# Performance work log

Measured on AMD Instinct MI355X. Metric: run time of the kernel, lower is better.

## Reference

```python
import jax, jax.numpy as jnp
import numpy as np

B, L, D = 32, 512, 128          # batch, seq_len, d_model (= num graph nodes N)
E, HS, DTR, U = 64, 64, 4, 32   # d_proj_E, d_proj_H (state), dt_rank, d_proj_U
R, K, DE, NH = 3, 3, 10, 4      # mamba layers, cheb order, d_e, heads
EPS = 1e-5


def _ln(x, g, b):
    m = jnp.mean(x, -1, keepdims=True)
    v = jnp.mean((x - m) ** 2, -1, keepdims=True)
    return (x - m) / jnp.sqrt(v + EPS) * g + b


def _mamba(x, in_w, conv_w, conv_b, xproj_w, dt_w, dt_b, Alog, Dp, out_w):
    b, l, _ = x.shape
    xz = x @ in_w                                  # (b,l,2E)
    xp, res = xz[..., :E], xz[..., E:]
    xc = jnp.transpose(xp, (0, 2, 1))              # (b,E,l)
    # causal depthwise conv: torch pads both sides by d_conv-1 then slices [:l]
    xc = jax.lax.conv_general_dilated(
        xc, conv_w, (1,), [(conv_w.shape[-1] - 1, 0)],
        dimension_numbers=('NCH', 'OIH', 'NCH'), feature_group_count=E)
    xc = xc + conv_b[None, :, None]
    xp = jax.nn.silu(jnp.transpose(xc, (0, 2, 1)))  # (b,l,E)
    xdbl = xp @ xproj_w                             # (b,l,DTR+2*HS)
    delta = jax.nn.softplus(xdbl[..., :DTR] @ dt_w + dt_b)        # (b,l,E)
    Bm = xdbl[..., DTR:DTR + HS]                                   # (b,l,HS)
    Cm = xdbl[..., DTR + HS:]                                      # (b,l,HS)
    A = -jnp.exp(Alog)                                             # (E,HS)
    dA = jnp.exp(delta[..., None] * A)                             # (b,l,E,HS)
    dBu = delta[..., None] * Bm[:, :, None, :] * xp[..., None]     # (b,l,E,HS)

    def step(s, t):
        dA_t, dBu_t, C_t = t
        s = dA_t * s + dBu_t
        return s, jnp.einsum('bdn,bn->bd', s, C_t)

    _, ys = jax.lax.scan(step, jnp.zeros((b, E, HS), x.dtype),
                         (jnp.swapaxes(dA, 0, 1), jnp.swapaxes(dBu, 0, 1),
                          jnp.swapaxes(Cm, 0, 1)))
    y = jnp.swapaxes(ys, 0, 1) + xp * Dp
    y = y * jax.nn.sigmoid(res)
    return y @ out_w


def _forward(x, mb_in_w, mb_conv_w, mb_conv_b, mb_xproj_w, mb_dt_w, mb_dt_b,
             mb_Alog, mb_D, mb_out_w, ln1_g, ln1_b, ln2_g, ln2_b,
             ffn_w1, ffn_b1, ffn_w2, ffn_b2,
             psi_emb, psi, W_q, W_k, attn_alpha, F_w, f_b, head_mix,
             head_w, head_b):
    # ---- bidirectional Mamba stack ----
    for i in range(R):
        f, bk = 2 * i, 2 * i + 1
        Y1 = _mamba(x, mb_in_w[f], mb_conv_w[f], mb_conv_b[f], mb_xproj_w[f],
                    mb_dt_w[f], mb_dt_b[f], mb_Alog[f], mb_D[f], mb_out_w[f])
        Y2 = jnp.flip(_mamba(jnp.flip(x, 1), mb_in_w[bk], mb_conv_w[bk],
                             mb_conv_b[bk], mb_xproj_w[bk], mb_dt_w[bk],
                             mb_dt_b[bk], mb_Alog[bk], mb_D[bk], mb_out_w[bk]), 1)
        Y3 = _ln(x + Y1 + Y2, ln1_g[i], ln1_b[i])
        Yp = jax.nn.relu(Y3 @ ffn_w1[i] + ffn_b1[i]) @ ffn_w2[i] + ffn_b2[i]
        x = _ln(Yp + Y3, ln2_g[i], ln2_b[i])
    h = jnp.transpose(x, (0, 2, 1))                # (B, N=D, L)
    # ---- MAGAC (deterministic single MC sample, eval, no edge drop) ----
    diff = psi_emb[:, None, :] - psi_emb[None, :, :]
    A_g = jax.nn.softmax(jnp.exp(-psi * jnp.sum(diff * diff, -1)), axis=1)
    Q = jnp.einsum('nd,dhm->nhm', psi_emb, W_q)
    Kt = jnp.einsum('nd,dhm->nhm', psi_emb, W_k)
    attn = jax.nn.softmax(jnp.einsum('nhd,mhd->hnm', Q, Kt)
                          / jnp.sqrt(jnp.asarray(DE, x.dtype)), axis=-1)
    alpha = jax.nn.sigmoid(attn_alpha)
    A_effs = alpha * A_g[None] + (1.0 - alpha) * attn   # (H,N,N)
    mix = jax.nn.softmax(head_mix)
    I = jnp.eye(D, dtype=x.dtype)
    out = jnp.zeros((x.shape[0], D), x.dtype)
    for hh in range(NH):
        A = A_effs[hh]
        sup = [I, A]
        for _ in range(2, K + 1):
            sup.append(2.0 * A @ sup[-1] - sup[-2])
        S = jnp.stack(sup, 0)                             # (K+1,N,N)
        Wf = jnp.einsum('nd,dkl->nkl', psi_emb, F_w[hh])  # (N,K+1,L)
        bf = psi_emb @ f_b[hh]                            # (N,)
        out_h = jnp.einsum('knm,bml,nkl->bn', S, h, Wf) + bf
        out = out + mix[hh] * out_h
    log_var = jnp.zeros_like(out)
    pred = out @ head_w + head_b                          # (B,1)
    return pred, log_var


def setup_inputs() -> dict:
    key = jax.random.key(0)
    ks = iter(jax.random.split(key, 40))
    nrm = lambda shp, s=0.05: (jax.random.normal(next(ks), shp, jnp.float32) * s)
    M = 2 * R
    base_Alog = jnp.log(jnp.arange(1, HS + 1, dtype=jnp.float32))
    inp = {
        'x': jax.random.normal(next(ks), (B, L, D), jnp.float32),
        'mb_in_w': nrm((M, D, 2 * E)),
        'mb_conv_w': nrm((M, E, 1, 3), 0.2),
        'mb_conv_b': jnp.zeros((M, E), jnp.float32),
        'mb_xproj_w': nrm((M, E, DTR + 2 * HS)),
        'mb_dt_w': nrm((M, DTR, E), 0.2),
        'mb_dt_b': jnp.zeros((M, E), jnp.float32),
        'mb_Alog': jnp.tile(base_Alog[None, None, :], (M, E, 1)),
        'mb_D': jnp.ones((M, E), jnp.float32),
        'mb_out_w': nrm((M, E, D)),
        'ln1_g': jnp.ones((R, D), jnp.float32),
        'ln1_b': jnp.zeros((R, D), jnp.float32),
        'ln2_g': jnp.ones((R, D), jnp.float32),
        'ln2_b': jnp.zeros((R, D), jnp.float32),
        'ffn_w1': nrm((R, D, U)),
        'ffn_b1': jnp.zeros((R, U), jnp.float32),
        'ffn_w2': nrm((R, U, D)),
        'ffn_b2': jnp.zeros((R, D), jnp.float32),
        'psi_emb': jax.random.normal(next(ks), (D, DE), jnp.float32),
        'psi': jnp.asarray(1.0, jnp.float32),
        'W_q': jax.random.normal(next(ks), (DE, NH, DE), jnp.float32),
        'W_k': jax.random.normal(next(ks), (DE, NH, DE), jnp.float32),
        'attn_alpha': jnp.asarray(0.5, jnp.float32),
        'F_w': nrm((NH, DE, K + 1, L), 0.05),
        'f_b': nrm((NH, DE), 1.0),
        'head_mix': jnp.ones((NH,), jnp.float32),
        'head_w': nrm((D, 1)),
        'head_b': jnp.zeros((1,), jnp.float32),
    }
    return inp


def reference(x, mb_in_w, mb_conv_w, mb_conv_b, mb_xproj_w, mb_dt_w, mb_dt_b,
              mb_Alog, mb_D, mb_out_w, ln1_g, ln1_b, ln2_g, ln2_b,
              ffn_w1, ffn_b1, ffn_w2, ffn_b2,
              psi_emb, psi, W_q, W_k, attn_alpha, F_w, f_b, head_mix,
              head_w, head_b):
    return _forward(x, mb_in_w, mb_conv_w, mb_conv_b, mb_xproj_w, mb_dt_w,
                    mb_dt_b, mb_Alog, mb_D, mb_out_w, ln1_g, ln1_b, ln2_g,
                    ln2_b, ffn_w1, ffn_b1, ffn_w2, ffn_b2, psi_emb, psi,
                    W_q, W_k, attn_alpha, F_w, f_b, head_mix, head_w, head_b)
```

## Files before the change

kernel.cpp:

```cpp
#include <hip/hip_runtime.h>
#include <hip/hip_bf16.h>


#define B_ 32
#define L_ 512
#define D_ 128
#define E_ 64
#define HS_ 64

#define OFF_X     0u
#define OFF_XZF   2097152u
#define OFF_XZB   4194304u
#define OFF_XPF   6291456u
#define OFF_XPB   7340032u
#define OFF_PKF   8388608u
#define OFF_PKB   10485760u
#define OFF_XBCF  12582912u
#define OFF_XBCB  14680064u
#define OFF_YSF   16777216u
#define OFF_YSB   17825792u
#define OFF_V     2097152u
#define OFF_WFT   10485760u
#define OFF_STT   11534336u
#define OFF_AEFF  11796480u
#define OFF_PART  12582912u
#define OFF_RED1  16777216u

__device__ __forceinline__ float sigf(float x) { return 1.f / (1.f + __expf(-x)); }
__device__ __forceinline__ unsigned int bf16r(float x) {
    unsigned int u = __float_as_uint(x);
    return (u + 0x7fffu + ((u >> 16) & 1u)) >> 16;
}

__global__ __launch_bounds__(256) void gemm_in2_kernel(
    const float* __restrict__ X, const float* __restrict__ WF, const float* __restrict__ WB,
    float* __restrict__ xzF, float* __restrict__ xzB)
{
    __shared__ float sxT[128][36];
    __shared__ float sw[2][16][128];
    const int tid = threadIdx.x;
    const int r0 = blockIdx.x * 32;
    for (int q = tid; q < 1024; q += 256) {
        const int r = q >> 5, k4 = q & 31;
        const float4 v = *(const float4*)&X[(size_t)(r0 + r) * 128 + k4 * 4];
        sxT[k4 * 4 + 0][r] = v.x; sxT[k4 * 4 + 1][r] = v.y;
        sxT[k4 * 4 + 2][r] = v.z; sxT[k4 * 4 + 3][r] = v.w;
    }
    const int wv = tid >> 6, lane = tid & 63;
    const int d = wv >> 1, ch = wv & 1;
    const int r4 = lane >> 4, c16 = lane & 15;
    float4 acc[8];
#pragma unroll
    for (int j = 0; j < 8; ++j) acc[j] = float4{0.f, 0.f, 0.f, 0.f};
    for (int ko = 0; ko < 128; ko += 16) {
        __syncthreads();
        for (int q = tid; q < 1024; q += 256) {
            const int dd = q >> 9, kk = (q >> 5) & 15, c4 = q & 31;
            *(float4*)&sw[dd][kk][c4 * 4] =
                *(const float4*)&((dd ? WB : WF)[(ko + kk) * 128 + c4 * 4]);
        }
        __syncthreads();
#pragma unroll
        for (int kk = 0; kk < 16; ++kk) {
            const float4 w4 = *(const float4*)&sw[d][kk][ch * 64 + c16 * 4];
            const float4 xa = *(const float4*)&sxT[ko + kk][r4 * 8];
            const float4 xb = *(const float4*)&sxT[ko + kk][r4 * 8 + 4];
            const float xs[8] = {xa.x, xa.y, xa.z, xa.w, xb.x, xb.y, xb.z, xb.w};
#pragma unroll
            for (int j = 0; j < 8; ++j) {
                acc[j].x = fmaf(xs[j], w4.x, acc[j].x);
                acc[j].y = fmaf(xs[j], w4.y, acc[j].y);
                acc[j].z = fmaf(xs[j], w4.z, acc[j].z);
                acc[j].w = fmaf(xs[j], w4.w, acc[j].w);
            }
        }
    }
    float* xz = d ? xzB : xzF;
#pragma unroll
    for (int j = 0; j < 8; ++j) {
        *(float4*)&xz[(r0 + r4 * 8 + j) * 128 + ch * 64 + c16 * 4] = acc[j];
    }
}

__global__ __launch_bounds__(256) void prep4_kernel(
    const float* __restrict__ xzF_, const float* __restrict__ xzB_,
    const float* __restrict__ conv_w, const float* __restrict__ conv_b,
    const float* __restrict__ xproj_w, const float* __restrict__ dt_w,
    const float* __restrict__ dt_b, int layer,
    float* __restrict__ xpF_, float* __restrict__ xpB_,
    unsigned int* __restrict__ xbcF_, unsigned int* __restrict__ xbcB_,
    float* __restrict__ pkF_, float* __restrict__ pkB_)
{
    __shared__ float sW[8448];
    __shared__ float sxp4[4][64][4];
    __shared__ float sdl4[4][4][4];
    const int tid = threadIdx.x, wv = tid >> 6, lane = tid & 63;
    const int dir = (int)(blockIdx.x >= 1024);
    const int r0 = (blockIdx.x & 1023) * 16;
    const int b = r0 >> 9;
    const int m = layer * 2 + dir;
    const float* Wg = xproj_w + m * 8448;
    for (int q = tid; q < 2112; q += 256) ((float4*)sW)[q] = ((const float4*)Wg)[q];
    const float* xz = dir ? xzB_ : xzF_;
    float* xp  = dir ? xpB_  : xpF_;
    unsigned int* xbc = dir ? xbcB_ : xbcF_;
    float* pkx = dir ? pkB_  : pkF_;
    const float* cw = conv_w + m * 192 + lane * 3;
    const float cw0 = cw[0], cw1 = cw[1], cw2 = cw[2];
    const float cb  = conv_b[m * 64 + lane];
    const float dtb = dt_b[m * 64 + lane];
    const float* dwp = dt_w + m * 256;
    const float dw0 = dwp[lane], dw1 = dwp[64 + lane], dw2 = dwp[128 + lane], dw3 = dwp[192 + lane];
    float uu[4];
#pragma unroll
    for (int it = 0; it < 4; ++it) {
        const int row = r0 + wv * 4 + it;
        const int l = row & 511;
        const int l1 = dir ? l + 1 : l - 1;
        const int l2 = dir ? l + 2 : l - 2;
        float acc = cb;
        const float x0 = xz[(size_t)row * 128 + lane];
        const float x1 = (l1 >= 0 && l1 < 512) ? xz[(size_t)(b * 512 + l1) * 128 + lane] : 0.f;
        const float x2 = (l2 >= 0 && l2 < 512) ? xz[(size_t)(b * 512 + l2) * 128 + lane] : 0.f;
        acc += cw0 * x2 + cw1 * x1 + cw2 * x0;
        const float u = acc * sigf(acc);
        xp[row * 64 + lane] = u;
        uu[it] = u;
    }
    *(float4*)&sxp4[wv][lane][0] = float4{uu[0], uu[1], uu[2], uu[3]};
    __syncthreads();
    const int jdt = lane & 3;
    float aB[4] = {0.f, 0.f, 0.f, 0.f};
    float aC[4] = {0.f, 0.f, 0.f, 0.f};
    float adt[4] = {0.f, 0.f, 0.f, 0.f};
#pragma unroll 4
    for (int k = 0; k < 64; ++k) {
        const float wB = sW[k * 132 + 4 + lane];
        const float wC = sW[k * 132 + 68 + lane];
        const float wd = sW[k * 132 + jdt];
        const float4 xv = *(const float4*)&sxp4[wv][k][0];
        aB[0] = fmaf(xv.x, wB, aB[0]); aC[0] = fmaf(xv.x, wC, aC[0]); adt[0] = fmaf(xv.x, wd, adt[0]);
        aB[1] = fmaf(xv.y, wB, aB[1]); aC[1] = fmaf(xv.y, wC, aC[1]); adt[1] = fmaf(xv.y, wd, adt[1]);
        aB[2] = fmaf(xv.z, wB, aB[2]); aC[2] = fmaf(xv.z, wC, aC[2]); adt[2] = fmaf(xv.z, wd, adt[2]);
        aB[3] = fmaf(xv.w, wB, aB[3]); aC[3] = fmaf(xv.w, wC, aC[3]); adt[3] = fmaf(xv.w, wd, adt[3]);
    }
#pragma unroll
    for (int it = 0; it < 4; ++it) {
        const int row = r0 + wv * 4 + it;
        xbc[row * 64 + lane] = (bf16r(aC[it]) << 16) | bf16r(aB[it]);
        if (lane < 4) sdl4[wv][it][lane] = adt[it];
    }
#pragma unroll
    for (int it = 0; it < 4; ++it) {
        const int row = r0 + wv * 4 + it;
        float dpre = fmaf(sdl4[wv][it][0], dw0, dtb);
        dpre = fmaf(sdl4[wv][it][1], dw1, dpre);
        dpre = fmaf(sdl4[wv][it][2], dw2, dpre);
        dpre = fmaf(sdl4[wv][it][3], dw3, dpre);
        const float dlt = (dpre > 20.f) ? dpre : log1pf(__expf(dpre));
        ((float2*)pkx)[row * 64 + lane] = float2{dlt, dlt * uu[it]};
    }
}

__global__ __launch_bounds__(256, 4) void scan8_kernel(
    const unsigned int* __restrict__ xbcF, const unsigned int* __restrict__ xbcB,
    const float* __restrict__ pkF, const float* __restrict__ pkB,
    const float* __restrict__ AlogF, const float* __restrict__ AlogB,
    float* __restrict__ ysF, float* __restrict__ ysB)
{
    __shared__ unsigned int sbc[2][1024];
    __shared__ float spk[2][4][16][2];
    __shared__ float ytile[4][16][68];
    const int tid = threadIdx.x, wv = tid >> 6, lane = tid & 63;
    const int bx = blockIdx.x;
    const int db = bx & 63;
    const int dir = db >> 5;
    const int b   = db & 31;
    const int e0  = (bx >> 6) * 4;
    const int e   = e0 + wv;
    const unsigned int* xbc = dir ? xbcB : xbcF;
    const float* pk  = dir ? pkB  : pkF;
    const float* Aw  = dir ? AlogB : AlogF;
    float* ys = dir ? ysB : ysF;
    const float a2 = -__expf(Aw[e * 64 + lane]) * 1.4426950408889634f;
    float s = 0.f;
    float* yrow = ys + (size_t)(b * 64 + e) * 512;

    const int psl = tid & 15, pw_ = tid >> 4;

#define STG_LOAD(RS)                                                              \
    {                                                                             \
        nb = *(const uint4*)(xbc + (size_t)(RS) * 64 + tid * 4);                  \
        if (tid < 64)                                                             \
            npp = *(const float2*)(pk + (size_t)((RS) + psl) * 128 + (e0 + pw_) * 2); \
    }
#define STG_WRITE(BUF)                                                            \
    {                                                                             \
        *(uint4*)(&sbc[BUF][tid * 4]) = nb;                                       \
        if (tid < 64) *(float2*)(&spk[BUF][pw_][psl][0]) = npp;                   \
    }

#define SCAN16(REV)                                                               \
    {                                                                             \
        const unsigned int* bc = &sbc[cur][0];                                    \
        const float* pq = &spk[cur][wv][0][0];                                    \
        _Pragma("unroll")                                                         \
        for (int j = 0; j < 8; ++j) {                                             \
            const int pj = (REV) ? 7 - j : j;                                     \
            const float4 pk4 = *(const float4*)(pq + pj * 4);                     \
            const int sA = (REV) ? 15 - 2 * j : 2 * j;                            \
            const int sB = (REV) ? 14 - 2 * j : 2 * j + 1;                        \
            const float dlA = (REV) ? pk4.z : pk4.x;                              \
            const float duA = (REV) ? pk4.w : pk4.y;                              \
            const float dlB = (REV) ? pk4.x : pk4.z;                              \
            const float duB = (REV) ? pk4.y : pk4.w;                              \
            const unsigned int bA = bc[sA * 64 + lane];                           \
            const float BnA = __uint_as_float(bA << 16);                          \
            const float CnA = __uint_as_float(bA & 0xffff0000u);                  \
            s = fmaf(__builtin_amdgcn_exp2f(dlA * a2), s, duA * BnA);             \
            ytile[wv][2 * j][lane] = s * CnA;                                     \
            const unsigned int bB = bc[sB * 64 + lane];                           \
            const float BnB = __uint_as_float(bB << 16);                          \
            const float CnB = __uint_as_float(bB & 0xffff0000u);                  \
            s = fmaf(__builtin_amdgcn_exp2f(dlB * a2), s, duB * BnB);             \
            ytile[wv][2 * j + 1][lane] = s * CnB;                                 \
        }                                                                         \
    }

    {
        uint4 nb; float2 npp;
        const int rs0 = b * 512 + (dir ? 496 : 0);
        STG_LOAD(rs0);
        STG_WRITE(0);
    }
    __syncthreads();

    int cur = 0;
    const int rr = lane & 15, sg = lane >> 4;
    for (int t = 0; t < 32; ++t) {
        uint4 nb; float2 npp;
        const bool more = (t + 1) < 32;
        if (more) {
            const int rs = b * 512 + (dir ? (496 - (t + 1) * 16) : ((t + 1) * 16));
            STG_LOAD(rs);
        }
        if (dir == 0) { SCAN16(0) } else { SCAN16(1) }
        {
            const float* yt = &ytile[wv][rr][sg * 16];
            const float4 A0 = *(const float4*)yt;
            const float4 A1 = *(const float4*)(yt + 4);
            const float4 A2 = *(const float4*)(yt + 8);
            const float4 A3 = *(const float4*)(yt + 12);
            float p = ((A0.x + A0.y) + (A0.z + A0.w)) + ((A1.x + A1.y) + (A1.z + A1.w))
                    + ((A2.x + A2.y) + (A2.z + A2.w)) + ((A3.x + A3.y) + (A3.z + A3.w));
            p += __shfl_xor(p, 16);
            p += __shfl_xor(p, 32);
            if (lane < 16) {
                const int lg = dir ? (511 - (t * 16 + rr)) : (t * 16 + rr);
                yrow[lg] = p;
            }
        }
        if (more) STG_WRITE(cur ^ 1);
        __syncthreads();
        cur ^= 1;
    }
#undef STG_LOAD
#undef STG_WRITE
#undef SCAN16
}

__global__ __launch_bounds__(256) void opfn2_kernel(
    const float* __restrict__ ysF, const float* __restrict__ ysB,
    const float* __restrict__ xpF, const float* __restrict__ xpB,
    const float* __restrict__ xzF, const float* __restrict__ xzB,
    const float* __restrict__ Dp, int layer,
    const float* __restrict__ Xc, const float* __restrict__ out_w,
    const float* __restrict__ W1, const float* __restrict__ b1,
    const float* __restrict__ W2, const float* __restrict__ b2,
    const float* __restrict__ g1, const float* __restrict__ bb1,
    const float* __restrict__ g2, const float* __restrict__ bb2,
    float* __restrict__ xout,
    const float* __restrict__ WFn, const float* __restrict__ WBn,
    float* __restrict__ xzFo, float* __restrict__ xzBo)
{
    __shared__ float smem[8832];
    float* syt = smem;
    float* y3  = smem;
    float* sy  = smem + 2176;
    float* sw  = smem + 4224;
    float* sh  = smem + 8320;
    const int tid = threadIdx.x;
    const int r0 = blockIdx.x * 16;
    const int b = r0 >> 9, l0 = r0 & 511;

    for (int q = tid; q < 512; q += 256) {
        const int d = q >> 8, ee = (q >> 2) & 63, rq = q & 3;
        const float* ysp = d ? ysB : ysF;
        const float4 v = *(const float4*)&ysp[(size_t)(b * 64 + ee) * 512 + l0 + rq * 4];
        float* dst = &syt[(d * 64 + ee) * 17 + rq * 4];
        dst[0] = v.x; dst[1] = v.y; dst[2] = v.z; dst[3] = v.w;
    }
    __syncthreads();
    for (int q = tid; q < 2048; q += 256) {
        const int r = q >> 7, c = q & 127;
        const int d = c >> 6, ee = c & 63;
        const int row = r0 + r;
        const float dv  = Dp[(layer * 2 + d) * 64 + ee];
        const float u   = (d ? xpB : xpF)[(size_t)row * 64 + ee];
        const float res = (d ? xzB : xzF)[(size_t)row * 128 + 64 + ee];
        sy[r * 128 + c] = (syt[(d * 64 + ee) * 17 + r] + u * dv) * sigf(res);
    }
    const int wv = tid >> 6, lane = tid & 63;
    const float* WFp = out_w + (layer * 2) * 8192;
    const float* WBp = out_w + (layer * 2 + 1) * 8192;
    float acc[4][2];
#pragma unroll
    for (int r = 0; r < 4; ++r) { acc[r][0] = 0.f; acc[r][1] = 0.f; }
    for (int ko = 0; ko < 128; ko += 32) {
        __syncthreads();
        for (int q = tid; q < 1024; q += 256) {
            const int kk = q >> 5, c4 = q & 31;
            const int kg = ko + kk;
            *(float4*)&sw[kk * 128 + c4 * 4] = (kg < 64)
                ? *(const float4*)&WFp[kg * 128 + c4 * 4]
                : *(const float4*)&WBp[(kg - 64) * 128 + c4 * 4];
        }
        __syncthreads();
#define OPSTEP(SRC, COMP, J)                                                      \
        {                                                                         \
            const float w0 = sw[(kk + (J)) * 128 + lane];                         \
            const float w1 = sw[(kk + (J)) * 128 + lane + 64];                    \
            acc[0][0] = fmaf(y40.COMP, w0, acc[0][0]);                            \
            acc[0][1] = fmaf(y40.COMP, w1, acc[0][1]);                            \
            acc[1][0] = fmaf(y41.COMP, w0, acc[1][0]);                            \
            acc[1][1] = fmaf(y41.COMP, w1, acc[1][1]);                            \
            acc[2][0] = fmaf(y42.COMP, w0, acc[2][0]);                            \
            acc[2][1] = fmaf(y42.COMP, w1, acc[2][1]);                            \
            acc[3][0] = fmaf(y43.COMP, w0, acc[3][0]);                            \
            acc[3][1] = fmaf(y43.COMP, w1, acc[3][1]);                            \
        }
#pragma unroll
        for (int kk = 0; kk < 32; kk += 4) {
            const float4 y40 = *(const float4*)&sy[(wv * 4 + 0) * 128 + ko + kk];
            const float4 y41 = *(const float4*)&sy[(wv * 4 + 1) * 128 + ko + kk];
            const float4 y42 = *(const float4*)&sy[(wv * 4 + 2) * 128 + ko + kk];
            const float4 y43 = *(const float4*)&sy[(wv * 4 + 3) * 128 + ko + kk];
            OPSTEP(sy, x, 0) OPSTEP(sy, y, 1) OPSTEP(sy, z, 2) OPSTEP(sy, w, 3)
        }
    }
    __syncthreads();
    for (int q = tid; q < 1024; q += 256) ((float4*)sw)[q] = ((const float4*)W1)[q];
#pragma unroll
    for (int r = 0; r < 4; ++r) {
        const int rl = wv * 4 + r;
        const int row = r0 + rl;
        float v0 = acc[r][0] + Xc[(size_t)row * 128 + lane];
        float v1 = acc[r][1] + Xc[(size_t)row * 128 + lane + 64];
        float sum = v0 + v1, sq = v0 * v0 + v1 * v1;
#pragma unroll
        for (int o = 32; o >= 1; o >>= 1) { sum += __shfl_xor(sum, o); sq += __shfl_xor(sq, o); }
        const float mean = sum * (1.f / 128.f);
        const float var = sq * (1.f / 128.f) - mean * mean;
        const float rs = rsqrtf(var + 1e-5f);
        y3[rl * 128 + lane]      = (v0 - mean) * rs * g1[lane] + bb1[lane];
        y3[rl * 128 + lane + 64] = (v1 - mean) * rs * g1[lane + 64] + bb1[lane + 64];
    }
    __syncthreads();
    {
        const int r = tid >> 4, u = tid & 15;
        float h0 = b1[u], h1 = b1[u + 16];
#pragma unroll 8
        for (int k = 0; k < 128; ++k) {
            const float xv = y3[r * 128 + k];
            h0 = fmaf(xv, sw[k * 32 + u], h0);
            h1 = fmaf(xv, sw[k * 32 + u + 16], h1);
        }
        sh[r * 32 + u]      = fmaxf(h0, 0.f);
        sh[r * 32 + u + 16] = fmaxf(h1, 0.f);
    }
    __syncthreads();
    for (int q = tid; q < 1024; q += 256) ((float4*)sw)[q] = ((const float4*)W2)[q];
    __syncthreads();
    float xr[4][2];
#pragma unroll
    for (int r = 0; r < 4; ++r) {
        const int rl = wv * 4 + r;
        float a0 = b2[lane], a1 = b2[lane + 64];
#pragma unroll 8
        for (int k = 0; k < 32; ++k) {
            const float hv = sh[rl * 32 + k];
            a0 = fmaf(hv, sw[k * 128 + lane], a0);
            a1 = fmaf(hv, sw[k * 128 + lane + 64], a1);
        }
        const float v0 = a0 + y3[rl * 128 + lane];
        const float v1 = a1 + y3[rl * 128 + lane + 64];
        float sum = v0 + v1, sq = v0 * v0 + v1 * v1;
#pragma unroll
        for (int o = 32; o >= 1; o >>= 1) { sum += __shfl_xor(sum, o); sq += __shfl_xor(sq, o); }
        const float mean = sum * (1.f / 128.f);
        const float var = sq * (1.f / 128.f) - mean * mean;
        const float rs = rsqrtf(var + 1e-5f);
        const int row = r0 + rl;
        const float o0 = (v0 - mean) * rs * g2[lane] + bb2[lane];
        const float o1 = (v1 - mean) * rs * g2[lane + 64] + bb2[lane + 64];
        xout[(size_t)row * 128 + lane]      = o0;
        xout[(size_t)row * 128 + lane + 64] = o1;
        xr[r][0] = o0; xr[r][1] = o1;
    }
    if (WFn == nullptr) return;
    __syncthreads();
    float* sxr = y3;
#pragma unroll
    for (int r = 0; r < 4; ++r) {
        sxr[(wv * 4 + r) * 128 + lane]      = xr[r][0];
        sxr[(wv * 4 + r) * 128 + lane + 64] = xr[r][1];
    }
    for (int d = 0; d < 2; ++d) {
        const float* Wn = d ? WBn : WFn;
        float* xzo = d ? xzBo : xzFo;
#pragma unroll
        for (int r = 0; r < 4; ++r) { acc[r][0] = 0.f; acc[r][1] = 0.f; }
        for (int ko = 0; ko < 128; ko += 32) {
            __syncthreads();
            for (int q = tid; q < 1024; q += 256) {
                const int kk = q >> 5, c4 = q & 31;
                *(float4*)&sw[kk * 128 + c4 * 4] = *(const float4*)&Wn[(ko + kk) * 128 + c4 * 4];
            }
            __syncthreads();
#pragma unroll
            for (int kk = 0; kk < 32; kk += 4) {
                const float4 y40 = *(const float4*)&sxr[(wv * 4 + 0) * 128 + ko + kk];
                const float4 y41 = *(const float4*)&sxr[(wv * 4 + 1) * 128 + ko + kk];
                const float4 y42 = *(const float4*)&sxr[(wv * 4 + 2) * 128 + ko + kk];
                const float4 y43 = *(const float4*)&sxr[(wv * 4 + 3) * 128 + ko + kk];
                OPSTEP(sxr, x, 0) OPSTEP(sxr, y, 1) OPSTEP(sxr, z, 2) OPSTEP(sxr, w, 3)
            }
        }
#pragma unroll
        for (int r = 0; r < 4; ++r) {
            const int row = r0 + wv * 4 + r;
            xzo[(size_t)row * 128 + lane]      = acc[r][0];
            xzo[(size_t)row * 128 + lane + 64] = acc[r][1];
        }
    }
#undef OPSTEP
}

__global__ __launch_bounds__(256) void head_wfqk_kernel(
    const float* __restrict__ psi, const float* __restrict__ F_w, float* __restrict__ WfT,
    const float* __restrict__ psis, const float* __restrict__ W_q, const float* __restrict__ W_k,
    const float* __restrict__ attn_a,
    float* __restrict__ Aeff, float* __restrict__ StT)
{
    __shared__ float sQ[2][10];
    __shared__ float red[2][128];
    if (blockIdx.x < 4096) {
        const int idx = blockIdx.x * 256 + threadIdx.x;
        const int n = idx & 127, l = (idx >> 7) & 511, k = (idx >> 16) & 3, h = idx >> 18;
        float acc = 0.f;
#pragma unroll
        for (int d = 0; d < 10; ++d)
            acc = fmaf(psi[n * 10 + d], F_w[((h * 10 + d) * 4 + k) * 512 + l], acc);
        WfT[idx] = acc;
        return;
    }
    const int q = blockIdx.x - 4096;
    const int half = threadIdx.x >> 7, mcol = threadIdx.x & 127;
    const int unit = q * 2 + half;
    const int h = unit >> 7, n = unit & 127;
    float Kreg[10];
#pragma unroll
    for (int d = 0; d < 10; ++d) Kreg[d] = 0.f;
#pragma unroll
    for (int d0 = 0; d0 < 10; ++d0) {
        const float pv = psi[mcol * 10 + d0];
#pragma unroll
        for (int d = 0; d < 10; ++d) Kreg[d] = fmaf(pv, W_k[(d0 * 4 + h) * 10 + d], Kreg[d]);
    }
    if (mcol < 10) {
        float qd = 0.f;
        for (int d0 = 0; d0 < 10; ++d0)
            qd = fmaf(psi[n * 10 + d0], W_q[(d0 * 4 + h) * 10 + mcol], qd);
        sQ[half][mcol] = qd;
    }
    __syncthreads();
    float d2 = 0.f;
#pragma unroll
    for (int d = 0; d < 10; ++d) { const float df = psi[n * 10 + d] - psi[mcol * 10 + d]; d2 = fmaf(df, df, d2); }
    const float gv = __expf(-psis[0] * d2);
    float qv = 0.f;
#pragma unroll
    for (int d = 0; d < 10; ++d) qv = fmaf(sQ[half][d], Kreg[d], qv);
    qv *= 0.3162277660168379332f;
    float* rd = red[half];
    float r;
    rd[mcol] = gv; __syncthreads();
    for (int s = 64; s >= 1; s >>= 1) { if (mcol < s) rd[mcol] = fmaxf(rd[mcol], rd[mcol + s]); __syncthreads(); }
    r = rd[0]; __syncthreads();
    const float eg = __expf(gv - r);
    rd[mcol] = eg; __syncthreads();
    for (int s = 64; s >= 1; s >>= 1) { if (mcol < s) rd[mcol] += rd[mcol + s]; __syncthreads(); }
    const float gsum = rd[0]; __syncthreads();
    rd[mcol] = qv; __syncthreads();
    for (int s = 64; s >= 1; s >>= 1) { if (mcol < s) rd[mcol] = fmaxf(rd[mcol], rd[mcol + s]); __syncthreads(); }
    r = rd[0]; __syncthreads();
    const float eq = __expf(qv - r);
    rd[mcol] = eq; __syncthreads();
    for (int s = 64; s >= 1; s >>= 1) { if (mcol < s) rd[mcol] += rd[mcol + s]; __syncthreads(); }
    const float qsum = rd[0];
    const float al = sigf(attn_a[0]);
    const float aeff = al * (eg / gsum) + (1.f - al) * (eq / qsum);
    Aeff[h * 16384 + n * 128 + mcol] = aeff;
    StT[((h * 4 + 1) * 128 + mcol) * 128 + n] = aeff;
    StT[((h * 4 + 0) * 128 + mcol) * 128 + n] = (mcol == n) ? 1.f : 0.f;
}

__global__ __launch_bounds__(256) void head_cheb_kernel(
    const float* __restrict__ Aeff, float* __restrict__ StT, int kk)
{
    const int h = blockIdx.x >> 6;
    const int m0 = ((blockIdx.x & 63) << 1) + (threadIdx.x >> 7);
    const int n = threadIdx.x & 127;
    const float* Ar = Aeff + h * 16384 + n * 128;
    const float* Sp = StT + ((h * 4 + kk - 1) * 128 + m0) * 128;
    float acc = 0.f;
#pragma unroll 8
    for (int p = 0; p < 128; ++p) acc = fmaf(Ar[p], Sp[p], acc);
    const float s2 = StT[((h * 4 + kk - 2) * 128 + m0) * 128 + n];
    StT[((h * 4 + kk) * 128 + m0) * 128 + n] = 2.f * acc - s2;
}

__global__ __launch_bounds__(256) void head_v4_kernel(
    const float* __restrict__ StT, const float* __restrict__ WfT, const float* __restrict__ hmix,
    float* __restrict__ V)
{
    const float m0 = hmix[0], m1 = hmix[1], m2 = hmix[2], m3 = hmix[3];
    const float mxx = fmaxf(fmaxf(m0, m1), fmaxf(m2, m3));
    const float e0 = __expf(m0 - mxx), e1 = __expf(m1 - mxx), e2 = __expf(m2 - mxx), e3 = __expf(m3 - mxx);
    const float inv = 1.f / (e0 + e1 + e2 + e3);
    const float mixv[4] = {e0 * inv, e1 * inv, e2 * inv, e3 * inv};
    const int tid = threadIdx.x;
    const int lt = blockIdx.x & 63, mm = blockIdx.x >> 6;
    const int n4 = tid & 31, mh = tid >> 5;
    const int m = mm * 8 + mh;
    const int l0 = lt * 8, n0 = n4 * 4;
    float4 sv[16];
#pragma unroll
    for (int h = 0; h < 4; ++h) {
        const float mx = mixv[h];
#pragma unroll
        for (int k = 0; k < 4; ++k) {
            const float4 v = *(const float4*)&StT[(size_t)((h * 4 + k) * 128 + m) * 128 + n0];
            sv[h * 4 + k] = float4{v.x * mx, v.y * mx, v.z * mx, v.w * mx};
        }
    }
#pragma unroll
    for (int j = 0; j < 8; ++j) {
        const int l = l0 + j;
        float4 acc = {0.f, 0.f, 0.f, 0.f};
#pragma unroll
        for (int hk = 0; hk < 16; ++hk) {
            const float4 w = *(const float4*)&WfT[(size_t)(hk * 512 + l) * 128 + n0];
            acc.x = fmaf(sv[hk].x, w.x, acc.x);
            acc.y = fmaf(sv[hk].y, w.y, acc.y);
            acc.z = fmaf(sv[hk].z, w.z, acc.z);
            acc.w = fmaf(sv[hk].w, w.w, acc.w);
        }
        *(float4*)&V[(size_t)(l * 128 + m) * 128 + n0] = acc;
    }
}

__global__ __launch_bounds__(256) void head_ctr_kernel(
    const float* __restrict__ Xf, const float* __restrict__ V, float* __restrict__ partial)
{
    __shared__ float sx[32][128];
    const int l = blockIdx.x, tid = threadIdx.x;
    const int n = tid & 127, mh = tid >> 7;
    for (int q = tid; q < 1024; q += 256) {
        const int b = q >> 5, m4 = q & 31;
        *(float4*)&sx[b][m4 * 4] = *(const float4*)&Xf[(size_t)(b * 512 + l) * 128 + m4 * 4];
    }
    __syncthreads();
    float acc[32];
#pragma unroll
    for (int b = 0; b < 32; ++b) acc[b] = 0.f;
    const float* vp = V + (size_t)(l * 128 + mh * 64) * 128 + n;
    for (int mm = 0; mm < 64; ++mm) {
        const float v = vp[(size_t)mm * 128];
        const int m = mh * 64 + mm;
#pragma unroll
        for (int b = 0; b < 32; ++b) acc[b] = fmaf(sx[b][m], v, acc[b]);
    }
#pragma unroll
    for (int b = 0; b < 32; ++b)
        partial[(size_t)((l * 2 + mh) * 32 + b) * 128 + n] = acc[b];
}

__global__ __launch_bounds__(128) void head_red_kernel(
    const float* __restrict__ partial, float* __restrict__ red1)
{
    const int b = blockIdx.x >> 5, cs = blockIdx.x & 31, n = threadIdx.x;
    const float* p = partial + ((size_t)(cs * 32) * 32 + b) * 128 + n;
    float s = 0.f;
#pragma unroll 8
    for (int c = 0; c < 32; ++c) s += p[(size_t)c * 4096];
    red1[(b * 32 + cs) * 128 + n] = s;
}

__global__ __launch_bounds__(128) void head_out_kernel(
    const float* __restrict__ red1, const float* __restrict__ psi,
    const float* __restrict__ f_b, const float* __restrict__ hmix,
    const float* __restrict__ head_w, const float* __restrict__ head_b, float* __restrict__ out)
{
    __shared__ float red[128];
    const int b = blockIdx.x, n = threadIdx.x;
    const float m0 = hmix[0], m1 = hmix[1], m2 = hmix[2], m3 = hmix[3];
    const float mxx = fmaxf(fmaxf(m0, m1), fmaxf(m2, m3));
    const float e0 = __expf(m0 - mxx), e1 = __expf(m1 - mxx), e2 = __expf(m2 - mxx), e3 = __expf(m3 - mxx);
    const float inv = 1.f / (e0 + e1 + e2 + e3);
    const float mixv[4] = {e0 * inv, e1 * inv, e2 * inv, e3 * inv};
    float s = 0.f;
#pragma unroll
    for (int h = 0; h < 4; ++h) {
        float t = 0.f;
#pragma unroll
        for (int d = 0; d < 10; ++d) t = fmaf(psi[n * 10 + d], f_b[h * 10 + d], t);
        s = fmaf(mixv[h], t, s);
    }
#pragma unroll 8
    for (int cs = 0; cs < 32; ++cs) s += red1[(b * 32 + cs) * 128 + n];
    red[n] = s * head_w[n];
    __syncthreads();
    for (int st = 64; st >= 1; st >>= 1) { if (n < st) red[n] += red[n + st]; __syncthreads(); }
    if (n == 0) out[b] = red[0] + head_b[0];
    out[32 + b * 128 + n] = 0.f;
}

extern "C" void kernel_launch(void* const* d_in, const int* in_sizes, int n_in,
                              void* d_out, int out_size, void* d_ws, size_t ws_size,
                              hipStream_t stream) {
    const float* x_in    = (const float*)d_in[0];
    const float* in_w    = (const float*)d_in[1];
    const float* conv_w  = (const float*)d_in[2];
    const float* conv_b  = (const float*)d_in[3];
    const float* xproj_w = (const float*)d_in[4];
    const float* dt_w    = (const float*)d_in[5];
    const float* dt_b    = (const float*)d_in[6];
    const float* Alog    = (const float*)d_in[7];
    const float* Dp      = (const float*)d_in[8];
    const float* out_w   = (const float*)d_in[9];
    const float* ln1_g   = (const float*)d_in[10];
    const float* ln1_b   = (const float*)d_in[11];
    const float* ln2_g   = (const float*)d_in[12];
    const float* ln2_b   = (const float*)d_in[13];
    const float* ffn_w1  = (const float*)d_in[14];
    const float* ffn_b1  = (const float*)d_in[15];
    const float* ffn_w2  = (const float*)d_in[16];
    const float* ffn_b2  = (const float*)d_in[17];
    const float* psi_emb = (const float*)d_in[18];
    const float* psi_s   = (const float*)d_in[19];
    const float* W_q     = (const float*)d_in[20];
    const float* W_k     = (const float*)d_in[21];
    const float* attn_a  = (const float*)d_in[22];
    const float* F_w     = (const float*)d_in[23];
    const float* f_b     = (const float*)d_in[24];
    const float* hmix    = (const float*)d_in[25];
    const float* head_w  = (const float*)d_in[26];
    const float* head_b  = (const float*)d_in[27];
    float* ws = (float*)d_ws;
    float* outp = (float*)d_out;

    gemm_in2_kernel<<<512, 256, 0, stream>>>(
        x_in, in_w, in_w + 16384, ws + OFF_XZF, ws + OFF_XZB);
    for (int i = 0; i < 3; ++i) {
        const float* xcur = (i == 0) ? x_in : (ws + OFF_X);
        const int mF = 2 * i, mB = 2 * i + 1;
        prep4_kernel<<<2048, 256, 0, stream>>>(
            ws + OFF_XZF, ws + OFF_XZB, conv_w, conv_b, xproj_w, dt_w, dt_b, i,
            ws + OFF_XPF, ws + OFF_XPB,
            (unsigned int*)(ws + OFF_XBCF), (unsigned int*)(ws + OFF_XBCB),
            ws + OFF_PKF, ws + OFF_PKB);
        scan8_kernel<<<1024, 256, 0, stream>>>(
            (const unsigned int*)(ws + OFF_XBCF), (const unsigned int*)(ws + OFF_XBCB),
            ws + OFF_PKF, ws + OFF_PKB,
            Alog + mF * 4096, Alog + mB * 4096, ws + OFF_YSF, ws + OFF_YSB);
        const float* WFn = (i < 2) ? (in_w + (2 * i + 2) * 16384) : nullptr;
        const float* WBn = (i < 2) ? (in_w + (2 * i + 3) * 16384) : nullptr;
        opfn2_kernel<<<1024, 256, 0, stream>>>(
            ws + OFF_YSF, ws + OFF_YSB, ws + OFF_XPF, ws + OFF_XPB, ws + OFF_XZF, ws + OFF_XZB,
            Dp, i, xcur, out_w,
            ffn_w1 + i * 4096, ffn_b1 + i * 32, ffn_w2 + i * 4096, ffn_b2 + i * 128,
            ln1_g + i * 128, ln1_b + i * 128, ln2_g + i * 128, ln2_b + i * 128,
            ws + OFF_X, WFn, WBn, ws + OFF_XZF, ws + OFF_XZB);
    }
    head_wfqk_kernel<<<4352, 256, 0, stream>>>(
        psi_emb, F_w, ws + OFF_WFT, psi_s, W_q, W_k, attn_a,
        ws + OFF_AEFF, ws + OFF_STT);
    head_cheb_kernel<<<256, 256, 0, stream>>>(ws + OFF_AEFF, ws + OFF_STT, 2);
    head_cheb_kernel<<<256, 256, 0, stream>>>(ws + OFF_AEFF, ws + OFF_STT, 3);
    head_v4_kernel<<<1024, 256, 0, stream>>>(ws + OFF_STT, ws + OFF_WFT, hmix, ws + OFF_V);
    head_ctr_kernel<<<512, 256, 0, stream>>>(ws + OFF_X, ws + OFF_V, ws + OFF_PART);
    head_red_kernel<<<1024, 128, 0, stream>>>(ws + OFF_PART, ws + OFF_RED1);
    head_out_kernel<<<32, 128, 0, stream>>>(
        ws + OFF_RED1, psi_emb, f_b, hmix, head_w, head_b, outp);
}
```

Baseline: 506.1 us.

## Process 32 rows per block in fused out-proj/FFN kernel to halve weight reloads

The fused out-projection, LayerNorm, FFN and next-layer in-projection kernel now handles 32 rows per block instead of 16, so each wave computes 8 rows and every weight tile staged in shared memory is reused twice as much. The launch drops from 1024 to 512 blocks. The gating prologue is fused into a single pass, the FFN first layer gives each thread 4 outputs, and the two next-layer GEMMs are merged into one chunk loop. The cost is more registers per thread (a 16-entry accumulator with an occupancy hint of 4), fewer blocks to spread across CUs, and slightly more shared memory. The scan kernel also gets small index rewrites.

```diff
diff --git a/kernel.cpp b/kernel.cpp
--- a/kernel.cpp
+++ b/kernel.cpp
@@ -218,12 +218,12 @@
             const float BnA = __uint_as_float(bA << 16);                          \
             const float CnA = __uint_as_float(bA & 0xffff0000u);                  \
             s = fmaf(__builtin_amdgcn_exp2f(dlA * a2), s, duA * BnA);             \
-            ytile[wv][2 * j][lane] = s * CnA;                                     \
+            ytile[wv][sA][lane] = s * CnA;                                        \
             const unsigned int bB = bc[sB * 64 + lane];                           \
             const float BnB = __uint_as_float(bB << 16);                          \
             const float CnB = __uint_as_float(bB & 0xffff0000u);                  \
             s = fmaf(__builtin_amdgcn_exp2f(dlB * a2), s, duB * BnB);             \
-            ytile[wv][2 * j + 1][lane] = s * CnB;                                 \
+            ytile[wv][sB][lane] = s * CnB;                                        \
         }                                                                         \
     }
 
@@ -256,7 +256,7 @@
             p += __shfl_xor(p, 16);
             p += __shfl_xor(p, 32);
             if (lane < 16) {
-                const int lg = dir ? (511 - (t * 16 + rr)) : (t * 16 + rr);
+                const int lg = dir ? (496 + rr - t * 16) : (t * 16 + rr);
                 yrow[lg] = p;
             }
         }
@@ -269,7 +269,7 @@
 #undef SCAN16
 }
 
-__global__ __launch_bounds__(256) void opfn2_kernel(
+__global__ __launch_bounds__(256, 4) void opfn3_kernel(
     const float* __restrict__ ysF, const float* __restrict__ ysB,
     const float* __restrict__ xpF, const float* __restrict__ xpB,
     const float* __restrict__ xzF, const float* __restrict__ xzB,
@@ -283,76 +283,82 @@
     const float* __restrict__ WFn, const float* __restrict__ WBn,
     float* __restrict__ xzFo, float* __restrict__ xzBo)
 {
-    __shared__ float smem[8832];
-    float* syt = smem;
-    float* y3  = smem;
-    float* sy  = smem + 2176;
-    float* sw  = smem + 4224;
-    float* sh  = smem + 8320;
+    __shared__ float smem[9216];
+    float* syy = smem;
+    float* sw  = smem + 4096;
+    float* sh  = smem + 8192;
     const int tid = threadIdx.x;
-    const int r0 = blockIdx.x * 16;
+    const int r0 = blockIdx.x * 32;
     const int b = r0 >> 9, l0 = r0 & 511;
-
-    for (int q = tid; q < 512; q += 256) {
-        const int d = q >> 8, ee = (q >> 2) & 63, rq = q & 3;
-        const float* ysp = d ? ysB : ysF;
-        const float4 v = *(const float4*)&ysp[(size_t)(b * 64 + ee) * 512 + l0 + rq * 4];
-        float* dst = &syt[(d * 64 + ee) * 17 + rq * 4];
-        dst[0] = v.x; dst[1] = v.y; dst[2] = v.z; dst[3] = v.w;
-    }
-    __syncthreads();
-    for (int q = tid; q < 2048; q += 256) {
-        const int r = q >> 7, c = q & 127;
-        const int d = c >> 6, ee = c & 63;
-        const int row = r0 + r;
-        const float dv  = Dp[(layer * 2 + d) * 64 + ee];
-        const float u   = (d ? xpB : xpF)[(size_t)row * 64 + ee];
-        const float res = (d ? xzB : xzF)[(size_t)row * 128 + 64 + ee];
-        sy[r * 128 + c] = (syt[(d * 64 + ee) * 17 + r] + u * dv) * sigf(res);
-    }
     const int wv = tid >> 6, lane = tid & 63;
     const float* WFp = out_w + (layer * 2) * 8192;
     const float* WBp = out_w + (layer * 2 + 1) * 8192;
-    float acc[4][2];
-#pragma unroll
-    for (int r = 0; r < 4; ++r) { acc[r][0] = 0.f; acc[r][1] = 0.f; }
-    for (int ko = 0; ko < 128; ko += 32) {
-        __syncthreads();
+
+    for (int q = tid; q < 1024; q += 256) {
+        const int d = q >> 9, ee = (q >> 3) & 63, rq = q & 7;
+        const float* ysp = d ? ysB : ysF;
+        const float4 v = *(const float4*)&ysp[(size_t)(b * 64 + ee) * 512 + l0 + rq * 4];
+        const float dv = Dp[(layer * 2 + d) * 64 + ee];
+        const float* xpp = d ? xpB : xpF;
+        const float* xzp = d ? xzB : xzF;
+        const float vv[4] = {v.x, v.y, v.z, v.w};
+#pragma unroll
+        for (int j = 0; j < 4; ++j) {
+            const int r = rq * 4 + j;
+            const int row = r0 + r;
+            const float u   = xpp[(size_t)row * 64 + ee];
+            const float res = xzp[(size_t)row * 128 + 64 + ee];
+            syy[r * 128 + d * 64 + ee] = (vv[j] + u * dv) * sigf(res);
+        }
+    }
+    __syncthreads();
+
+    float acc[8][2];
+#pragma unroll
+    for (int r = 0; r < 8; ++r) { acc[r][0] = 0.f; acc[r][1] = 0.f; }
+#define OPSTEP8(COMP, J)                                                          \
+        {                                                                         \
+            const float w0 = sw[(kk + (J)) * 128 + lane];                         \
+            const float w1 = sw[(kk + (J)) * 128 + lane + 64];                    \
+            acc[0][0] = fmaf(y40.COMP, w0, acc[0][0]); acc[0][1] = fmaf(y40.COMP, w1, acc[0][1]); \
+            acc[1][0] = fmaf(y41.COMP, w0, acc[1][0]); acc[1][1] = fmaf(y41.COMP, w1, acc[1][1]); \
+            acc[2][0] = fmaf(y42.COMP, w0, acc[2][0]); acc[2][1] = fmaf(y42.COMP, w1, acc[2][1]); \
+            acc[3][0] = fmaf(y43.COMP, w0, acc[3][0]); acc[3][1] = fmaf(y43.COMP, w1, acc[3][1]); \
+            acc[4][0] = fmaf(y44.COMP, w0, acc[4][0]); acc[4][1] = fmaf(y44.COMP, w1, acc[4][1]); \
+            acc[5][0] = fmaf(y45.COMP, w0, acc[5][0]); acc[5][1] = fmaf(y45.COMP, w1, acc[5][1]); \
+            acc[6][0] = fmaf(y46.COMP, w0, acc[6][0]); acc[6][1] = fmaf(y46.COMP, w1, acc[6][1]); \
+            acc[7][0] = fmaf(y47.COMP, w0, acc[7][0]); acc[7][1] = fmaf(y47.COMP, w1, acc[7][1]); \
+        }
+#define GEMM_CHUNK8(SRC, KO)                                                      \
+    _Pragma("unroll")                                                             \
+    for (int kk = 0; kk < 32; kk += 4) {                                          \
+        const float4 y40 = *(const float4*)&(SRC)[(wv * 8 + 0) * 128 + (KO) + kk];\
+        const float4 y41 = *(const float4*)&(SRC)[(wv * 8 + 1) * 128 + (KO) + kk];\
+        const float4 y42 = *(const float4*)&(SRC)[(wv * 8 + 2) * 128 + (KO) + kk];\
+        const float4 y43 = *(const float4*)&(SRC)[(wv * 8 + 3) * 128 + (KO) + kk];\
+        const float4 y44 = *(const float4*)&(SRC)[(wv * 8 + 4) * 128 + (KO) + kk];\
+        const float4 y45 = *(const float4*)&(SRC)[(wv * 8 + 5) * 128 + (KO) + kk];\
+        const float4 y46 = *(const float4*)&(SRC)[(wv * 8 + 6) * 128 + (KO) + kk];\
+        const float4 y47 = *(const float4*)&(SRC)[(wv * 8 + 7) * 128 + (KO) + kk];\
+        OPSTEP8(x, 0) OPSTEP8(y, 1) OPSTEP8(z, 2) OPSTEP8(w, 3)                  \
+    }
+    for (int koi = 0; koi < 4; ++koi) {
+        if (koi) __syncthreads();
         for (int q = tid; q < 1024; q += 256) {
             const int kk = q >> 5, c4 = q & 31;
-            const int kg = ko + kk;
+            const int kg = koi * 32 + kk;
             *(float4*)&sw[kk * 128 + c4 * 4] = (kg < 64)
                 ? *(const float4*)&WFp[kg * 128 + c4 * 4]
                 : *(const float4*)&WBp[(kg - 64) * 128 + c4 * 4];
         }
         __syncthreads();
-#define OPSTEP(SRC, COMP, J)                                                      \
-        {                                                                         \
-            const float w0 = sw[(kk + (J)) * 128 + lane];                         \
-            const float w1 = sw[(kk + (J)) * 128 + lane + 64];                    \
-            acc[0][0] = fmaf(y40.COMP, w0, acc[0][0]);                            \
-            acc[0][1] = fmaf(y40.COMP, w1, acc[0][1]);                            \
-            acc[1][0] = fmaf(y41.COMP, w0, acc[1][0]);                            \
-            acc[1][1] = fmaf(y41.COMP, w1, acc[1][1]);                            \
-            acc[2][0] = fmaf(y42.COMP, w0, acc[2][0]);                            \
-            acc[2][1] = fmaf(y42.COMP, w1, acc[2][1]);                            \
-            acc[3][0] = fmaf(y43.COMP, w0, acc[3][0]);                            \
-            acc[3][1] = fmaf(y43.COMP, w1, acc[3][1]);                            \
-        }
-#pragma unroll
-        for (int kk = 0; kk < 32; kk += 4) {
-            const float4 y40 = *(const float4*)&sy[(wv * 4 + 0) * 128 + ko + kk];
-            const float4 y41 = *(const float4*)&sy[(wv * 4 + 1) * 128 + ko + kk];
-            const float4 y42 = *(const float4*)&sy[(wv * 4 + 2) * 128 + ko + kk];
-            const float4 y43 = *(const float4*)&sy[(wv * 4 + 3) * 128 + ko + kk];
-            OPSTEP(sy, x, 0) OPSTEP(sy, y, 1) OPSTEP(sy, z, 2) OPSTEP(sy, w, 3)
-        }
+        GEMM_CHUNK8(syy, koi * 32);
     }
     __syncthreads();
     for (int q = tid; q < 1024; q += 256) ((float4*)sw)[q] = ((const float4*)W1)[q];
 #pragma unroll
-    for (int r = 0; r < 4; ++r) {
-        const int rl = wv * 4 + r;
+    for (int r = 0; r < 8; ++r) {
+        const int rl = wv * 8 + r;
         const int row = r0 + rl;
         float v0 = acc[r][0] + Xc[(size_t)row * 128 + lane];
         float v1 = acc[r][1] + Xc[(size_t)row * 128 + lane + 64];
@@ -362,29 +368,33 @@
         const float mean = sum * (1.f / 128.f);
         const float var = sq * (1.f / 128.f) - mean * mean;
         const float rs = rsqrtf(var + 1e-5f);
-        y3[rl * 128 + lane]      = (v0 - mean) * rs * g1[lane] + bb1[lane];
-        y3[rl * 128 + lane + 64] = (v1 - mean) * rs * g1[lane + 64] + bb1[lane + 64];
+        syy[rl * 128 + lane]      = (v0 - mean) * rs * g1[lane] + bb1[lane];
+        syy[rl * 128 + lane + 64] = (v1 - mean) * rs * g1[lane + 64] + bb1[lane + 64];
     }
     __syncthreads();
     {
-        const int r = tid >> 4, u = tid & 15;
-        float h0 = b1[u], h1 = b1[u + 16];
+        const int r = tid >> 3, ug = (tid & 7) * 4;
+        float h0 = b1[ug], h1 = b1[ug + 1], h2 = b1[ug + 2], h3 = b1[ug + 3];
 #pragma unroll 8
         for (int k = 0; k < 128; ++k) {
-            const float xv = y3[r * 128 + k];
-            h0 = fmaf(xv, sw[k * 32 + u], h0);
-            h1 = fmaf(xv, sw[k * 32 + u + 16], h1);
-        }
-        sh[r * 32 + u]      = fmaxf(h0, 0.f);
-        sh[r * 32 + u + 16] = fmaxf(h1, 0.f);
+            const float xv = syy[r * 128 + k];
+            h0 = fmaf(xv, sw[k * 32 + ug], h0);
+            h1 = fmaf(xv, sw[k * 32 + ug + 1], h1);
+            h2 = fmaf(xv, sw[k * 32 + ug + 2], h2);
+            h3 = fmaf(xv, sw[k * 32 + ug + 3], h3);
+        }
+        sh[r * 32 + ug]     = fmaxf(h0, 0.f);
+        sh[r * 32 + ug + 1] = fmaxf(h1, 0.f);
+        sh[r * 32 + ug + 2] = fmaxf(h2, 0.f);
+        sh[r * 32 + ug + 3] = fmaxf(h3, 0.f);
     }
     __syncthreads();
     for (int q = tid; q < 1024; q += 256) ((float4*)sw)[q] = ((const float4*)W2)[q];
     __syncthreads();
-    float xr[4][2];
-#pragma unroll
-    for (int r = 0; r < 4; ++r) {
-        const int rl = wv * 4 + r;
+    float xr[8][2];
+#pragma unroll
+    for (int r = 0; r < 8; ++r) {
+        const int rl = wv * 8 + r;
         float a0 = b2[lane], a1 = b2[lane + 64];
 #pragma unroll 8
         for (int k = 0; k < 32; ++k) {
@@ -392,8 +402,8 @@
             a0 = fmaf(hv, sw[k * 128 + lane], a0);
             a1 = fmaf(hv, sw[k * 128 + lane + 64], a1);
         }
-        const float v0 = a0 + y3[rl * 128 + lane];
-        const float v1 = a1 + y3[rl * 128 + lane + 64];
+        const float v0 = a0 + syy[rl * 128 + lane];
+        const float v1 = a1 + syy[rl * 128 + lane + 64];
         float sum = v0 + v1, sq = v0 * v0 + v1 * v1;
 #pragma unroll
         for (int o = 32; o >= 1; o >>= 1) { sum += __shfl_xor(sum, o); sq += __shfl_xor(sq, o); }
@@ -409,41 +419,38 @@
     }
     if (WFn == nullptr) return;
     __syncthreads();
-    float* sxr = y3;
-#pragma unroll
-    for (int r = 0; r < 4; ++r) {
-        sxr[(wv * 4 + r) * 128 + lane]      = xr[r][0];
-        sxr[(wv * 4 + r) * 128 + lane + 64] = xr[r][1];
-    }
-    for (int d = 0; d < 2; ++d) {
-        const float* Wn = d ? WBn : WFn;
-        float* xzo = d ? xzBo : xzFo;
-#pragma unroll
-        for (int r = 0; r < 4; ++r) { acc[r][0] = 0.f; acc[r][1] = 0.f; }
-        for (int ko = 0; ko < 128; ko += 32) {
-            __syncthreads();
-            for (int q = tid; q < 1024; q += 256) {
-                const int kk = q >> 5, c4 = q & 31;
-                *(float4*)&sw[kk * 128 + c4 * 4] = *(const float4*)&Wn[(ko + kk) * 128 + c4 * 4];
+    float* sxr = syy;
+#pragma unroll
+    for (int r = 0; r < 8; ++r) {
+        sxr[(wv * 8 + r) * 128 + lane]      = xr[r][0];
+        sxr[(wv * 8 + r) * 128 + lane + 64] = xr[r][1];
+    }
+    for (int c = 0; c < 8; ++c) {
+        const int dd = c >> 2, ko = (c & 3) * 32;
+        const float* Wn = dd ? WBn : WFn;
+        for (int q = tid; q < 1024; q += 256) {
+            const int kk = q >> 5, c4 = q & 31;
+            *(float4*)&sw[kk * 128 + c4 * 4] = *(const float4*)&Wn[(ko + kk) * 128 + c4 * 4];
+        }
+        __syncthreads();
+        if ((c & 3) == 0) {
+#pragma unroll
+            for (int r = 0; r < 8; ++r) { acc[r][0] = 0.f; acc[r][1] = 0.f; }
+        }
+        GEMM_CHUNK8(sxr, ko);
+        if ((c & 3) == 3) {
+            float* xzo = dd ? xzBo : xzFo;
+#pragma unroll
+            for (int r = 0; r < 8; ++r) {
+                const int row = r0 + wv * 8 + r;
+                xzo[(size_t)row * 128 + lane]      = acc[r][0];
+                xzo[(size_t)row * 128 + lane + 64] = acc[r][1];
             }
-            __syncthreads();
-#pragma unroll
-            for (int kk = 0; kk < 32; kk += 4) {
-                const float4 y40 = *(const float4*)&sxr[(wv * 4 + 0) * 128 + ko + kk];
-                const float4 y41 = *(const float4*)&sxr[(wv * 4 + 1) * 128 + ko + kk];
-                const float4 y42 = *(const float4*)&sxr[(wv * 4 + 2) * 128 + ko + kk];
-                const float4 y43 = *(const float4*)&sxr[(wv * 4 + 3) * 128 + ko + kk];
-                OPSTEP(sxr, x, 0) OPSTEP(sxr, y, 1) OPSTEP(sxr, z, 2) OPSTEP(sxr, w, 3)
-            }
-        }
-#pragma unroll
-        for (int r = 0; r < 4; ++r) {
-            const int row = r0 + wv * 4 + r;
-            xzo[(size_t)row * 128 + lane]      = acc[r][0];
-            xzo[(size_t)row * 128 + lane + 64] = acc[r][1];
-        }
-    }
-#undef OPSTEP
+        }
+        __syncthreads();
+    }
+#undef OPSTEP8
+#undef GEMM_CHUNK8
 }
 
 __global__ __launch_bounds__(256) void head_wfqk_kernel(
@@ -686,7 +693,7 @@
             Alog + mF * 4096, Alog + mB * 4096, ws + OFF_YSF, ws + OFF_YSB);
         const float* WFn = (i < 2) ? (in_w + (2 * i + 2) * 16384) : nullptr;
         const float* WBn = (i < 2) ? (in_w + (2 * i + 3) * 16384) : nullptr;
-        opfn2_kernel<<<1024, 256, 0, stream>>>(
+        opfn3_kernel<<<512, 256, 0, stream>>>(
             ws + OFF_YSF, ws + OFF_YSB, ws + OFF_XPF, ws + OFF_XPB, ws + OFF_XZF, ws + OFF_XZB,
             Dp, i, xcur, out_w,
             ffn_w1 + i * 4096, ffn_b1 + i * 32, ffn_w2 + i * 4096, ffn_b2 + i * 128,
```

Result: no change. 507.8 us (+0.3%).
